# Performance work log

Measured on AMD Instinct MI355X. Metric: run time of the kernel, lower is better.

Reference implementation:

```python
import jax, jax.numpy as jnp
import numpy as np

B, L, D, N, NBLK = 16, 2048, 256, 64, 6  # 6 S4D layers: blocks 1,2,3,5 + 2 inner layers of FS4Ddeq


def setup_inputs() -> dict:
    key = jax.random.key(0)
    ks = jax.random.split(key, 12)
    x = jax.random.normal(ks[0], (B, L), dtype=jnp.float32)
    W_emb = jax.random.normal(ks[1], (1, D), dtype=jnp.float32) * 0.1
    b_emb = jnp.zeros((D,), jnp.float32)
    # S4D parameters, stacked over the 6 layers
    log_dt = jax.random.uniform(ks[2], (NBLK, D), minval=float(np.log(1e-3)), maxval=float(np.log(1e-1)), dtype=jnp.float32)
    logAre = jnp.full((NBLK, D, N), float(np.log(0.5)), jnp.float32)
    Aim = jnp.broadcast_to(jnp.pi * jnp.arange(N, dtype=jnp.float32), (NBLK, D, N)) * jnp.ones((NBLK, D, N), jnp.float32)
    Cre = jax.random.normal(ks[3], (NBLK, D, N), dtype=jnp.float32) * (0.5 ** 0.5)
    Cim = jax.random.normal(ks[4], (NBLK, D, N), dtype=jnp.float32) * (0.5 ** 0.5)
    Dskip = jax.random.normal(ks[5], (NBLK, D), dtype=jnp.float32)
    Wout = jax.random.normal(ks[6], (NBLK, D, D), dtype=jnp.float32) / np.sqrt(D)
    bout = jnp.zeros((NBLK, D), jnp.float32)
    gamma = jnp.ones((NBLK, D), jnp.float32)
    beta = jnp.zeros((NBLK, D), jnp.float32)
    # feedforward of the FS4Ddeq block (feed_size=[B,L,emb_dim], feed_act='relu')
    feed_W1 = jax.random.normal(ks[7], (D, D), dtype=jnp.float32) / np.sqrt(D)
    feed_b1 = jnp.zeros((D,), jnp.float32)
    feed_W2 = jax.random.normal(ks[8], (D, D), dtype=jnp.float32) / np.sqrt(D)
    feed_b2 = jnp.zeros((D,), jnp.float32)
    fc_W = jax.random.normal(ks[9], (D, 2), dtype=jnp.float32) / np.sqrt(D)
    fc_b = jnp.zeros((2,), jnp.float32)
    return dict(x=x, W_emb=W_emb, b_emb=b_emb, log_dt=log_dt, logAre=logAre, Aim=Aim,
                Cre=Cre, Cim=Cim, Dskip=Dskip, Wout=Wout, bout=bout, gamma=gamma, beta=beta,
                feed_W1=feed_W1, feed_b1=feed_b1, feed_W2=feed_W2, feed_b2=feed_b2,
                fc_W=fc_W, fc_b=fc_b)


def _s4d_block(h, log_dt, logAre, Aim, Cre, Cim, Dskip, Wout, bout, gamma, beta):
    """Pre-norm (BN eval-mode) -> diagonal SSM (ZOH, FFT conv) -> GELU -> Linear -> residual."""
    _, Lh, _ = h.shape
    z = gamma * h + beta  # BatchNorm in eval mode with identity running stats
    dt = jnp.exp(log_dt)[:, None]                      # [D,1]
    A = -jnp.exp(logAre) + 1j * Aim                    # [D,N] diagonal state matrix
    dtA = dt * A                                       # [D,N]
    C = (Cre + 1j * Cim) * (jnp.exp(dtA) - 1.0) / A    # ZOH-discretized C*B
    # Vandermonde kernel K[d,l] = 2*Re sum_n C[d,n] * exp(dtA[d,n])^l
    vand = jnp.exp(dtA[:, :, None] * jnp.arange(Lh, dtype=jnp.float32))  # [D,N,L]
    K = 2.0 * jnp.einsum('dn,dnl->dl', C, vand).real   # [D,L]
    u = jnp.transpose(z, (0, 2, 1))                    # [B,D,L]
    kf = jnp.fft.rfft(K, n=2 * Lh)
    uf = jnp.fft.rfft(u, n=2 * Lh)
    y = jnp.fft.irfft(uf * kf, n=2 * Lh)[..., :Lh]     # causal conv
    y = y + Dskip[:, None] * u                         # feedthrough D
    y = jax.nn.gelu(jnp.transpose(y, (0, 2, 1)))       # [B,L,D]
    y = jnp.einsum('bld,de->ble', y, Wout) + bout      # output projection
    return y + h                                       # skip connection


def reference(x, W_emb, b_emb, log_dt, logAre, Aim, Cre, Cim, Dskip, Wout, bout,
              gamma, beta, feed_W1, feed_b1, feed_W2, feed_b2, fc_W, fc_b):
    h = x[..., None] @ W_emb + b_emb  # nn.Linear(1, emb_dim): [B,L,D]
    # layers 1,2,3,5: S4D blocks (dropout is identity in eval mode)
    for i in range(4):
        h = _s4d_block(h, log_dt[i], logAre[i], Aim[i], Cre[i], Cim[i],
                       Dskip[i], Wout[i], bout[i], gamma[i], beta[i])
    # layer4: FS4Ddeq_model with layers=2 inner S4D blocks + relu feed net + final relu + skip
    r = h
    for i in (4, 5):
        h = _s4d_block(h, log_dt[i], logAre[i], Aim[i], Cre[i], Cim[i],
                       Dskip[i], Wout[i], bout[i], gamma[i], beta[i])
    h = jax.nn.relu(h @ feed_W1 + feed_b1) @ feed_W2 + feed_b2
    h = jax.nn.relu(h + r)
    mean_y = jnp.mean(h, axis=1)       # [B,D]
    logits = mean_y @ fc_W + fc_b      # [B,2]
    return logits
```

## Files before the change

kernel.cpp:

```cpp
#include <hip/hip_runtime.h>
#include <hip/hip_fp16.h>
#include <math.h>

#define B_ 16
#define L_ 2048
#define D_ 256
#define N_ 64
#define NBLK_ 6
#define LC_ 128
#define NC_ 16

typedef _Float16 half8 __attribute__((ext_vector_type(8)));
typedef float f32x4 __attribute__((ext_vector_type(4)));

__device__ __forceinline__ unsigned short f2h(float f) {
  _Float16 h = (_Float16)f;
  return *(unsigned short*)&h;
}
__device__ __forceinline__ float h2f(unsigned short u) {
  _Float16 h = *(_Float16*)&u;
  return (float)h;
}

__global__ __launch_bounds__(256) void prep_kernel(
    const float* __restrict__ x, const float* __restrict__ wemb,
    const float* __restrict__ bemb,
    const float* __restrict__ log_dt, const float* __restrict__ logAre,
    const float* __restrict__ Aim, const float* __restrict__ Cre,
    const float* __restrict__ Cim,
    const float* __restrict__ Wout, const float* __restrict__ fW1,
    const float* __restrict__ fW2,
    float* __restrict__ wbuf, float* __restrict__ c2buf,
    float* __restrict__ wlbuf, unsigned short* __restrict__ WT,
    unsigned short* __restrict__ H, unsigned short* __restrict__ UT,
    int* __restrict__ cnt) {
  __shared__ __align__(16) unsigned char ldsraw[17408];
  int bid = blockIdx.x;
  int tid = threadIdx.x;
  if (bid < 384) {
    if (bid == 0 && tid < 16) cnt[tid] = 0;
    int idx = bid * 256 + tid;
    if (idx < NBLK_ * D_ * N_) {
      int blk = idx >> 14;
      int rem = idx & 16383;
      int d = rem >> 6;
      int n = rem & 63;
      float dt   = expf(log_dt[blk * D_ + d]);
      float are  = -expf(logAre[idx]);
      float aim  = Aim[idx];
      float dtar = dt * are, dtai = dt * aim;
      float er = expf(dtar);
      float wr = er * cosf(dtai);
      float wi = er * sinf(dtai);
      float inv = 1.0f / (are * are + aim * aim);
      float wm1r = wr - 1.0f;
      float br = (wm1r * are + wi * aim) * inv;
      float bi2 = (wi * are - wm1r * aim) * inv;
      float crv = Cre[idx], civ = Cim[idx];
      float c2r = 2.0f * (crv * br - civ * bi2);
      float c2i = 2.0f * (crv * bi2 + civ * br);
      float eL = expf((float)LC_ * dtar);
      float angL = (float)LC_ * dtai;
      float* wb = wbuf + (size_t)((blk << 8) + d) * 128;
      wb[n] = wr; wb[64 + n] = wi;
      float* cb = c2buf + (size_t)((blk << 8) + d) * 128;
      cb[n] = c2r; cb[64 + n] = c2i;
      wlbuf[2 * idx] = eL * cosf(angL); wlbuf[2 * idx + 1] = eL * sinf(angL);
    }
  } else if (bid < 512) {
    float (*tile)[65] = (float (*)[65])ldsraw;
    int b2 = bid - 384;
    int wv = b2 >> 4;
    int tk = (b2 >> 2) & 3;
    int tn = b2 & 3;
    const float* src = (wv < 6) ? (Wout + (size_t)wv * 65536) : (wv == 6 ? fW1 : fW2);
    int r = tid >> 4;
    int c = (tid & 15) << 2;
    for (int rr = 0; rr < 64; rr += 16) {
      float4 v = *(const float4*)(src + (size_t)(tk * 64 + r + rr) * 256 + tn * 64 + c);
      tile[r + rr][c] = v.x; tile[r + rr][c + 1] = v.y;
      tile[r + rr][c + 2] = v.z; tile[r + rr][c + 3] = v.w;
    }
    __syncthreads();
    for (int rr = 0; rr < 64; rr += 16) {
      int n = r + rr;
      ushort4 o;
      o.x = f2h(tile[c + 0][n]); o.y = f2h(tile[c + 1][n]);
      o.z = f2h(tile[c + 2][n]); o.w = f2h(tile[c + 3][n]);
      *(ushort4*)(WT + (size_t)wv * 65536 + (size_t)(tn * 64 + n) * 256 + tk * 64 + c) = o;
    }
  } else {
    unsigned short (*lds)[136] = (unsigned short (*)[136])ldsraw;
    int bi = bid - 512;
    int bc = bi >> 2, dq = bi & 3;
    int b = bc >> 4, ch = bc & 15;
    int tau0 = tid >> 4;
    int dl = (tid & 15) << 2;
    float w4[4], b4[4];
#pragma unroll
    for (int i = 0; i < 4; ++i) {
      w4[i] = wemb[dq * 64 + dl + i];
      b4[i] = bemb[dq * 64 + dl + i];
    }
    for (int tt = 0; tt < 128; tt += 16) {
      int l = ch * 128 + tt + tau0;
      float xv = x[b * L_ + l];
      ushort4 hv;
      float v0 = fmaf(xv, w4[0], b4[0]);
      float v1 = fmaf(xv, w4[1], b4[1]);
      float v2 = fmaf(xv, w4[2], b4[2]);
      float v3 = fmaf(xv, w4[3], b4[3]);
      hv.x = f2h(v0); hv.y = f2h(v1); hv.z = f2h(v2); hv.w = f2h(v3);
      lds[dl + 0][tt + tau0] = hv.x;
      lds[dl + 1][tt + tau0] = hv.y;
      lds[dl + 2][tt + tau0] = hv.z;
      lds[dl + 3][tt + tau0] = hv.w;
      *(ushort4*)(H + ((size_t)(b * L_ + l)) * D_ + dq * 64 + dl) = hv;
    }
    __syncthreads();
    int r = tid >> 2, seg = (tid & 3) << 5;
    unsigned short* dst = UT + ((size_t)((dq * 64 + r) * 256 + bc)) * 128 + seg;
    const unsigned short* srow = &lds[r][seg];
    *(uint4*)(dst + 0)  = *(const uint4*)(srow + 0);
    *(uint4*)(dst + 8)  = *(const uint4*)(srow + 8);
    *(uint4*)(dst + 16) = *(const uint4*)(srow + 16);
    *(uint4*)(dst + 24) = *(const uint4*)(srow + 24);
  }
}

__global__ __launch_bounds__(512) void scan_fused(
    const unsigned short* __restrict__ UT,
    const float* __restrict__ WB, const float* __restrict__ C2B,
    const float* __restrict__ WLB,
    const float* __restrict__ gamma_, const float* __restrict__ beta_,
    const float* __restrict__ dskip,
    unsigned short* __restrict__ GT, int blk) {
  __shared__ __align__(16) unsigned short SLl[256 * 136];
  __shared__ __align__(16) unsigned short Bm1[128 * 136];
  __shared__ __align__(16) unsigned short Bm2[128 * 136];
  __shared__ float wc[256];
  __shared__ float Kt[128];
  __shared__ float Pb[128];
  __shared__ float Sb[128];
  int d = blockIdx.x;
  int tid = threadIdx.x, lane = tid & 63, w = tid >> 6;
  int wm = (w & 3) << 6;
  int wn = (w >> 2) << 6;
  int cn = lane & 15, rq = lane >> 4;
  int ko = rq << 3;
  const unsigned short* Au = UT + (size_t)d * 256 * 128;

  half8 afr[4][4];
#pragma unroll
  for (int kc2 = 0; kc2 < 4; ++kc2)
#pragma unroll
    for (int mf = 0; mf < 4; ++mf)
      afr[kc2][mf] = *(const half8*)(Au + (size_t)(wm + (mf << 4) + cn) * 128 + (kc2 << 5) + ko);

  if (tid < 128) wc[tid] = WB[(size_t)((blk << 8) + d) * 128 + tid];
  else if (tid < 256) wc[tid] = C2B[(size_t)((blk << 8) + d) * 128 + (tid - 128)];
  __syncthreads();
  int n = tid & 63;
  float gd = gamma_[blk * D_ + d], bd = beta_[blk * D_ + d], dsk = dskip[blk * D_ + d];
  {
    float wr = wc[n], wi = wc[64 + n];
    float c2r = wc[128 + n], c2i = wc[192 + n];
    int j0 = w << 4;
    float pr = 1.f, pi = 0.f, br = wr, bi = wi;
    int e = j0;
    while (e) {
      if (e & 1) { float tt = pr * br - pi * bi; pi = pr * bi + pi * br; pr = tt; }
      float t2 = br * br - bi * bi; bi = 2.f * br * bi; br = t2;
      e >>= 1;
    }
    for (int k2 = 0; k2 < 16; ++k2) {
      int j = j0 + k2;
      Bm1[n * 136 + (127 - j)]        = f2h(gd * pr);
      Bm1[(64 + n) * 136 + (127 - j)] = f2h(-gd * pi);
      float qr = pr * wr - pi * wi, qi = pr * wi + pi * wr;
      Bm2[j * 136 + n]      = f2h(c2r * qr - c2i * qi);
      Bm2[j * 136 + 64 + n] = f2h(c2r * qi + c2i * qr);
      float kc = c2r * pr - c2i * pi;
#pragma unroll
      for (int off = 1; off < 64; off <<= 1) kc += __shfl_xor(kc, off);
      if (n == 0) Kt[j] = kc + (j == 0 ? dsk : 0.f);
      pr = qr; pi = qi;
    }
  }
  if (tid < 64) {
    const float* wlp = WLB + (((size_t)((blk << 8) + d)) * 64 + tid) * 2;
    float wlr = wlp[0], wli = wlp[1];
    float nr = wlr - 1.f, ni = wli;
    float dr2 = wc[tid] - 1.f, di = wc[64 + tid];
    float iv = 1.f / (dr2 * dr2 + di * di);
    Sb[tid]      = bd * ((nr * dr2 + ni * di) * iv);
    Sb[64 + tid] = bd * (-((ni * dr2 - nr * di) * iv));
  }
  __syncthreads();

  {
    f32x4 acc[4][4];
#pragma unroll
    for (int a = 0; a < 4; ++a)
#pragma unroll
      for (int b2 = 0; b2 < 4; ++b2) acc[a][b2] = (f32x4){0.f, 0.f, 0.f, 0.f};
#pragma unroll
    for (int kc = 0; kc < 4; ++kc) {
      half8 bf4[4];
#pragma unroll
      for (int nf = 0; nf < 4; ++nf)
        bf4[nf] = *(const half8*)((const _Float16*)Bm1 + (wn + (nf << 4) + cn) * 136 + (kc << 5) + ko);
#pragma unroll
      for (int mf = 0; mf < 4; ++mf)
#pragma unroll
        for (int nf = 0; nf < 4; ++nf)
          acc[mf][nf] = __builtin_amdgcn_mfma_f32_16x16x32_f16(afr[kc][mf], bf4[nf], acc[mf][nf], 0, 0, 0);
    }
#pragma unroll
    for (int nf = 0; nf < 4; ++nf) {
      int nl = wn + (nf << 4) + cn;
      float sb = Sb[nl];
#pragma unroll
      for (int mf = 0; mf < 4; ++mf)
#pragma unroll
        for (int rr = 0; rr < 4; ++rr) {
          int row = wm + (mf << 4) + (rq << 2) + rr;
          SLl[row * 136 + nl] = f2h(acc[mf][nf][rr] + sb);
        }
    }
  }
  __syncthreads();

  if (tid < 128) {
    float ps = 0.f;
    for (int t2 = 0; t2 <= tid; ++t2) ps += Kt[t2];
    Pb[tid] = bd * ps;
  }
  for (int task = tid; task < 1024; task += 512) {
    int b = task >> 6, nn = task & 63;
    const float* wlp = WLB + (((size_t)((blk << 8) + d)) * 64 + nn) * 2;
    float wlr = wlp[0], wli = wlp[1];
    float Sr = 0.f, Sj = 0.f;
    int row0 = b << 4;
    float tr2 = h2f(SLl[row0 * 136 + nn]);
    float tj2 = h2f(SLl[row0 * 136 + 64 + nn]);
    for (int c = 0; c < NC_; ++c) {
      int row = row0 + c;
      float ntr = 0.f, ntj = 0.f;
      if (c < NC_ - 1) {
        ntr = h2f(SLl[(row + 1) * 136 + nn]);
        ntj = h2f(SLl[(row + 1) * 136 + 64 + nn]);
      }
      SLl[row * 136 + nn]      = f2h(Sr);
      SLl[row * 136 + 64 + nn] = f2h(Sj);
      float nSr = fmaf(wlr, Sr, fmaf(wli, Sj, tr2));
      Sj = fmaf(-wli, Sr, fmaf(wlr, Sj, tj2));
      Sr = nSr;
      tr2 = ntr; tj2 = ntj;
    }
  }
  __syncthreads();

  {
    int chunk = tid & 15, rg = tid >> 4;
#pragma unroll
    for (int it = 0; it < 4; ++it) {
      int trow = (it << 5) + rg;
      int tau0 = chunk << 3;
      unsigned short v[8];
#pragma unroll
      for (int i = 0; i < 8; ++i) {
        int tau = tau0 + i;
        v[i] = (tau <= trow) ? f2h(gd * Kt[trow - tau]) : (unsigned short)0;
      }
      *(uint4*)(Bm1 + (size_t)trow * 136 + tau0) = *(uint4*)v;
    }
  }
  __syncthreads();

  {
    f32x4 acc[4][4];
#pragma unroll
    for (int a = 0; a < 4; ++a)
#pragma unroll
      for (int b2 = 0; b2 < 4; ++b2) acc[a][b2] = (f32x4){0.f, 0.f, 0.f, 0.f};
#pragma unroll
    for (int kb = 0; kb < 8; ++kb) {
      int kc = (kb & 3) << 5;
      half8 af[4], bf4[4];
      if (kb < 4) {
#pragma unroll
        for (int mf = 0; mf < 4; ++mf) af[mf] = afr[kb][mf];
#pragma unroll
        for (int nf = 0; nf < 4; ++nf)
          bf4[nf] = *(const half8*)((const _Float16*)Bm1 + (wn + (nf << 4) + cn) * 136 + kc + ko);
      } else {
#pragma unroll
        for (int mf = 0; mf < 4; ++mf)
          af[mf] = *(const half8*)((const _Float16*)SLl + (wm + (mf << 4) + cn) * 136 + kc + ko);
#pragma unroll
        for (int nf = 0; nf < 4; ++nf)
          bf4[nf] = *(const half8*)((const _Float16*)Bm2 + (wn + (nf << 4) + cn) * 136 + kc + ko);
      }
#pragma unroll
      for (int mf = 0; mf < 4; ++mf)
#pragma unroll
        for (int nf = 0; nf < 4; ++nf)
          acc[mf][nf] = __builtin_amdgcn_mfma_f32_16x16x32_f16(af[mf], bf4[nf], acc[mf][nf], 0, 0, 0);
    }
    __syncthreads();
    unsigned short* epi = SLl;
#pragma unroll
    for (int nf = 0; nf < 4; ++nf) {
      int nl = wn + (nf << 4) + cn;
      float pb2 = Pb[nl];
#pragma unroll
      for (int mf = 0; mf < 4; ++mf)
#pragma unroll
        for (int rr = 0; rr < 4; ++rr) {
          int ml = wm + (mf << 4) + (rq << 2) + rr;
          float xx = acc[mf][nf][rr] + pb2;
          float x3 = xx * xx * xx;
          float inner = 0.7978845608028654f * fmaf(0.044715f, x3, xx);
          float e = __expf(-2.f * fabsf(inner));
          float th = (1.f - e) / (1.f + e);
          th = copysignf(th, inner);
          epi[ml * 136 + nl] = f2h(0.5f * xx * (1.f + th));
        }
    }
    __syncthreads();
    int mr = tid >> 1, hf = (tid & 1) << 6;
    size_t gb = ((size_t)d * 256 + mr) * 128 + hf;
#pragma unroll
    for (int k = 0; k < 8; ++k)
      *(uint4*)(GT + gb + k * 8) = *(const uint4*)&epi[mr * 136 + hf + k * 8];
  }
}

__global__ __launch_bounds__(256, 4) void gemm_gt(const unsigned short* __restrict__ GT,
    const unsigned short* __restrict__ Wt, const float* __restrict__ bias,
    const unsigned short* __restrict__ res, unsigned short* __restrict__ hout,
    unsigned short* __restrict__ ut_next) {
  __shared__ __align__(16) unsigned short smem[9216 + 4608];
  unsigned short* As = smem;
  unsigned short* Bs = smem + 9216;
  int tid = threadIdx.x;
  int bid = blockIdx.x;
  int bc = bid & 255;
  int m0 = bc << 7, n0 = (bid >> 8) << 6;
  int lane = tid & 63, w = tid >> 6;
  int wm = (w & 1) << 6, wn = (w >> 1) << 5;
  int rb = tid >> 3, cb = (tid & 7) << 3;
  int dr = tid >> 2, sg = (tid & 3) << 5;
  f32x4 acc[4][2];
#pragma unroll
  for (int mf = 0; mf < 4; ++mf)
#pragma unroll
    for (int nf = 0; nf < 2; ++nf) acc[mf][nf] = (f32x4){0.f, 0.f, 0.f, 0.f};

  uint4 gv[4], bv[2];
  {
    const uint4* grow = (const uint4*)(GT + ((size_t)(dr * 256 + bc)) * 128 + sg);
    gv[0] = grow[0]; gv[1] = grow[1]; gv[2] = grow[2]; gv[3] = grow[3];
#pragma unroll
    for (int rr = 0; rr < 2; ++rr)
      bv[rr] = *(const uint4*)(Wt + (size_t)(n0 + rb + rr * 32) * 256 + cb);
  }
  for (int kb = 0; kb < 4; ++kb) {
    __syncthreads();
    const unsigned short* pv = (const unsigned short*)gv;
#pragma unroll
    for (int i = 0; i < 32; ++i) As[(sg + i) * 72 + dr] = pv[i];
#pragma unroll
    for (int rr = 0; rr < 2; ++rr) *(uint4*)&Bs[(rb + rr * 32) * 72 + cb] = bv[rr];
    __syncthreads();
    if (kb < 3) {
      int k0 = (kb + 1) << 6;
      const uint4* grow = (const uint4*)(GT + ((size_t)((k0 + dr) * 256 + bc)) * 128 + sg);
      gv[0] = grow[0]; gv[1] = grow[1]; gv[2] = grow[2]; gv[3] = grow[3];
#pragma unroll
      for (int rr = 0; rr < 2; ++rr)
        bv[rr] = *(const uint4*)(Wt + (size_t)(n0 + rb + rr * 32) * 256 + k0 + cb);
    }
#pragma unroll
    for (int kw = 0; kw < 2; ++kw) {
      int ko = (kw << 5) + ((lane >> 4) << 3);
      half8 af[4], bfr[2];
#pragma unroll
      for (int mf = 0; mf < 4; ++mf)
        af[mf] = *(const half8*)&As[(wm + (mf << 4) + (lane & 15)) * 72 + ko];
#pragma unroll
      for (int nf = 0; nf < 2; ++nf)
        bfr[nf] = *(const half8*)&Bs[(wn + (nf << 4) + (lane & 15)) * 72 + ko];
#pragma unroll
      for (int mf = 0; mf < 4; ++mf)
#pragma unroll
        for (int nf = 0; nf < 2; ++nf)
          acc[mf][nf] = __builtin_amdgcn_mfma_f32_16x16x32_f16(af[mf], bfr[nf], acc[mf][nf], 0, 0, 0);
    }
  }
  int cn = lane & 15, rq = lane >> 4;
  __syncthreads();
  unsigned short* epi = smem;
#pragma unroll
  for (int nf = 0; nf < 2; ++nf) {
    int nl = wn + (nf << 4) + cn;
    float bv2 = bias[n0 + nl];
#pragma unroll
    for (int mf = 0; mf < 4; ++mf)
#pragma unroll
      for (int r = 0; r < 4; ++r) {
        int ml = wm + (mf << 4) + (rq << 2) + r;
        float v = acc[mf][nf][r] + bv2 + h2f(res[(size_t)(m0 + ml) * 256 + n0 + nl]);
        epi[ml * 72 + nl] = f2h(v);
      }
  }
  __syncthreads();
  {
    int mr = tid >> 1, hf = (tid & 1) << 5;
    unsigned short* dst = hout + (size_t)(m0 + mr) * 256 + n0 + hf;
    const unsigned short* srow = epi + mr * 72 + hf;
#pragma unroll
    for (int k = 0; k < 4; ++k) *(uint4*)(dst + k * 8) = *(const uint4*)(srow + k * 8);
  }
  if (ut_next) {
    int nl = tid >> 2, sg2 = (tid & 3) << 5;
    unsigned short* dst = ut_next + ((size_t)(n0 + nl) * 256 + bc) * 128 + sg2;
#pragma unroll
    for (int k = 0; k < 4; ++k) {
      unsigned short v8[8];
#pragma unroll
      for (int e = 0; e < 8; ++e) v8[e] = epi[(sg2 + k * 8 + e) * 72 + nl];
      *(uint4*)(dst + k * 8) = *(uint4*)v8;
    }
  }
}

__global__ __launch_bounds__(256, 4) void gemm_ffn(const unsigned short* __restrict__ A,
    const unsigned short* __restrict__ Wt, const float* __restrict__ bias,
    const unsigned short* __restrict__ res, unsigned short* __restrict__ outp) {
  __shared__ __align__(16) unsigned short smem[9216 + 4608];
  unsigned short* As = smem;
  unsigned short* Bs = smem + 9216;
  int tid = threadIdx.x;
  int bid = blockIdx.x;
  int m0 = (bid & 255) << 7, n0 = (bid >> 8) << 6;
  int lane = tid & 63, w = tid >> 6;
  int wm = (w & 1) << 6, wn = (w >> 1) << 5;
  int r0 = tid >> 3;
  int c0 = (tid & 7) << 3;
  f32x4 acc[4][2];
#pragma unroll
  for (int mf = 0; mf < 4; ++mf)
#pragma unroll
    for (int nf = 0; nf < 2; ++nf) acc[mf][nf] = (f32x4){0.f, 0.f, 0.f, 0.f};

  uint4 av[4], bv[2];
#pragma unroll
  for (int rr = 0; rr < 4; ++rr)
    av[rr] = *(const uint4*)(A + (size_t)(m0 + r0 + rr * 32) * 256 + c0);
#pragma unroll
  for (int rr = 0; rr < 2; ++rr)
    bv[rr] = *(const uint4*)(Wt + (size_t)(n0 + r0 + rr * 32) * 256 + c0);
  for (int kb = 0; kb < 4; ++kb) {
    __syncthreads();
#pragma unroll
    for (int rr = 0; rr < 4; ++rr) *(uint4*)&As[(r0 + rr * 32) * 72 + c0] = av[rr];
#pragma unroll
    for (int rr = 0; rr < 2; ++rr) *(uint4*)&Bs[(r0 + rr * 32) * 72 + c0] = bv[rr];
    __syncthreads();
    if (kb < 3) {
      int k0 = (kb + 1) << 6;
#pragma unroll
      for (int rr = 0; rr < 4; ++rr)
        av[rr] = *(const uint4*)(A + (size_t)(m0 + r0 + rr * 32) * 256 + k0 + c0);
#pragma unroll
      for (int rr = 0; rr < 2; ++rr)
        bv[rr] = *(const uint4*)(Wt + (size_t)(n0 + r0 + rr * 32) * 256 + k0 + c0);
    }
#pragma unroll
    for (int kw = 0; kw < 2; ++kw) {
      int ko = (kw << 5) + ((lane >> 4) << 3);
      half8 af[4], bfr[2];
#pragma unroll
      for (int mf = 0; mf < 4; ++mf)
        af[mf] = *(const half8*)&As[(wm + (mf << 4) + (lane & 15)) * 72 + ko];
#pragma unroll
      for (int nf = 0; nf < 2; ++nf)
        bfr[nf] = *(const half8*)&Bs[(wn + (nf << 4) + (lane & 15)) * 72 + ko];
#pragma unroll
      for (int mf = 0; mf < 4; ++mf)
#pragma unroll
        for (int nf = 0; nf < 2; ++nf)
          acc[mf][nf] = __builtin_amdgcn_mfma_f32_16x16x32_f16(af[mf], bfr[nf], acc[mf][nf], 0, 0, 0);
    }
  }
  int cn = lane & 15, rq = lane >> 4;
  __syncthreads();
  unsigned short* epi = smem;
#pragma unroll
  for (int nf = 0; nf < 2; ++nf) {
    int nl = wn + (nf << 4) + cn;
#pragma unroll
    for (int r = 0; r < 4; ++r) {
#pragma unroll
      for (int mf = 0; mf < 4; ++mf) {
        int ml = wm + (mf << 4) + (rq << 2) + r;
        epi[ml * 72 + nl] = f2h(acc[mf][nf][r]);
      }
    }
  }
  __syncthreads();
  int mr = tid >> 1, hf = (tid & 1) << 5;
  unsigned short* dst = outp + (size_t)(m0 + mr) * 256 + n0 + hf;
#pragma unroll
  for (int k = 0; k < 4; ++k) {
    uint4 c = *(const uint4*)&epi[mr * 72 + hf + k * 8];
    uint4 rv = (uint4){0, 0, 0, 0};
    if (res) rv = *(const uint4*)(res + (size_t)(m0 + mr) * 256 + n0 + hf + k * 8);
    const unsigned short* cp = (const unsigned short*)&c;
    const unsigned short* rp = (const unsigned short*)&rv;
    unsigned short o8[8];
#pragma unroll
    for (int e = 0; e < 8; ++e) {
      float v = h2f(cp[e]) + bias[n0 + hf + k * 8 + e];
      if (res) v += h2f(rp[e]);
      o8[e] = f2h(fmaxf(v, 0.f));
    }
    *(uint4*)(dst + k * 8) = *(uint4*)o8;
  }
}

__global__ __launch_bounds__(256) void head_kernel(const unsigned short* __restrict__ H,
    float* __restrict__ part, int* __restrict__ cnt,
    const float* __restrict__ fcW, const float* __restrict__ fcb,
    float* __restrict__ out) {
  __shared__ float meanv[D_];
  __shared__ int lastFlag;
  int b = blockIdx.x, ls = blockIdx.y, d = threadIdx.x;
  const unsigned short* p = H + ((size_t)(b * L_ + ls * 128)) * D_ + d;
  float sum = 0.f;
  for (int l = 0; l < 128; ++l) sum += h2f(p[(size_t)l * D_]);
  part[(b * 16 + ls) * D_ + d] = sum;
  __syncthreads();
  if (d == 0) {
    __threadfence();
    lastFlag = (atomicAdd(&cnt[b], 1) == 15) ? 1 : 0;
  }
  __syncthreads();
  if (lastFlag) {
    __threadfence();
    const volatile float* vp = part;
    float s = 0.f;
    for (int i = 0; i < 16; ++i) s += vp[(b * 16 + i) * D_ + d];
    meanv[d] = s * (1.0f / (float)L_);
    __syncthreads();
    if (d < 2) {
      float accv = fcb[d];
      for (int k = 0; k < D_; ++k) accv = fmaf(meanv[k], fcW[k * 2 + d], accv);
      out[b * 2 + d] = accv;
    }
  }
}

extern "C" void kernel_launch(void* const* d_in, const int* in_sizes, int n_in,
                              void* d_out, int out_size, void* d_ws, size_t ws_size,
                              hipStream_t stream) {
  const float* x      = (const float*)d_in[0];
  const float* W_emb  = (const float*)d_in[1];
  const float* b_emb  = (const float*)d_in[2];
  const float* log_dt = (const float*)d_in[3];
  const float* logAre = (const float*)d_in[4];
  const float* Aim    = (const float*)d_in[5];
  const float* Cre    = (const float*)d_in[6];
  const float* Cim    = (const float*)d_in[7];
  const float* Dskip  = (const float*)d_in[8];
  const float* Wout   = (const float*)d_in[9];
  const float* bout   = (const float*)d_in[10];
  const float* gamma_ = (const float*)d_in[11];
  const float* beta_  = (const float*)d_in[12];
  const float* fW1    = (const float*)d_in[13];
  const float* fb1    = (const float*)d_in[14];
  const float* fW2    = (const float*)d_in[15];
  const float* fb2    = (const float*)d_in[16];
  const float* fcW    = (const float*)d_in[17];
  const float* fcb    = (const float*)d_in[18];
  float* outp = (float*)d_out;

  const size_t HSZ = (size_t)B_ * L_ * D_;
  float* WB     = (float*)d_ws;
  float* C2B    = WB + (size_t)NBLK_ * D_ * 128;
  float* WLB    = C2B + (size_t)NBLK_ * D_ * 128;
  unsigned short* H   = (unsigned short*)(WLB + (size_t)NBLK_ * D_ * N_ * 2);
  unsigned short* R   = H + HSZ;
  unsigned short* UT  = R + HSZ;
  unsigned short* GT  = UT + HSZ;
  unsigned short* Gbf = GT;
  unsigned short* WT  = GT + HSZ;
  int* cnt = (int*)(WT + (size_t)8 * 65536);

  prep_kernel<<<1536, 256, 0, stream>>>(x, W_emb, b_emb, log_dt, logAre, Aim, Cre, Cim,
                                        Wout, fW1, fW2, WB, C2B, WLB, WT, H, UT, cnt);

  const unsigned short* hin_t[6]  = {H, H, H, H, R, H};
  unsigned short*       hout_t[6] = {H, H, H, R, H, H};
  for (int i = 0; i < 6; ++i) {
    scan_fused<<<256, 512, 0, stream>>>(UT, WB, C2B, WLB, gamma_, beta_, Dskip, GT, i);
    gemm_gt<<<1024, 256, 0, stream>>>(
        GT, WT + (size_t)i * 65536, bout + i * D_, hin_t[i], hout_t[i],
        (i < 5) ? UT : nullptr);
  }
  gemm_ffn<<<1024, 256, 0, stream>>>(H, WT + (size_t)6 * 65536, fb1, nullptr, Gbf);
  gemm_ffn<<<1024, 256, 0, stream>>>(Gbf, WT + (size_t)7 * 65536, fb2, R, H);
  head_kernel<<<dim3(16, 16), 256, 0, stream>>>(H, WB, cnt, fcW, fcb, outp);
}
```

Before: 538.6 us.

## Split scan_fused across two blocks per channel to halve LDS and double grid

Each channel's 256-row chunk matrix is now processed by two workgroups, each handling 128 rows (half the batch). Shared memory drops by merging Bm1/Bm2 into one reused buffer and halving SLl, and the output GEMMs are reordered so the state-contribution product is computed before the causal Toeplitz matrix overwrites the buffer. This lets more workgroups fit per CU and doubles the grid from 256 to 512 blocks to fill the GPU better. The cost is that per-channel setup (the power series, the kernel taps and their prefix sums) is recomputed in both blocks. It also adds s_setprio around the MFMA loops and a launch-bounds occupancy hint.

```diff
diff --git a/kernel.cpp b/kernel.cpp
--- a/kernel.cpp
+++ b/kernel.cpp
@@ -128,27 +128,28 @@
   }
 }
 
-__global__ __launch_bounds__(512) void scan_fused(
+__global__ __launch_bounds__(512, 4) void scan_fused(
     const unsigned short* __restrict__ UT,
     const float* __restrict__ WB, const float* __restrict__ C2B,
     const float* __restrict__ WLB,
     const float* __restrict__ gamma_, const float* __restrict__ beta_,
     const float* __restrict__ dskip,
     unsigned short* __restrict__ GT, int blk) {
-  __shared__ __align__(16) unsigned short SLl[256 * 136];
-  __shared__ __align__(16) unsigned short Bm1[128 * 136];
-  __shared__ __align__(16) unsigned short Bm2[128 * 136];
+  __shared__ __align__(16) unsigned short SLl[128 * 136];
+  __shared__ __align__(16) unsigned short Bm[128 * 136];
   __shared__ float wc[256];
   __shared__ float Kt[128];
   __shared__ float Pb[128];
   __shared__ float Sb[128];
-  int d = blockIdx.x;
+  int bid = blockIdx.x;
+  int d = bid >> 1;
+  int hm = (bid & 1) << 7;
   int tid = threadIdx.x, lane = tid & 63, w = tid >> 6;
-  int wm = (w & 3) << 6;
-  int wn = (w >> 2) << 6;
+  int wm = (w & 1) << 6;
+  int wn = (w >> 1) << 5;
   int cn = lane & 15, rq = lane >> 4;
   int ko = rq << 3;
-  const unsigned short* Au = UT + (size_t)d * 256 * 128;
+  const unsigned short* Au = UT + ((size_t)d * 256 + hm) * 128;
 
   half8 afr[4][4];
 #pragma unroll
@@ -162,10 +163,11 @@
   __syncthreads();
   int n = tid & 63;
   float gd = gamma_[blk * D_ + d], bd = beta_[blk * D_ + d], dsk = dskip[blk * D_ + d];
-  {
-    float wr = wc[n], wi = wc[64 + n];
-    float c2r = wc[128 + n], c2i = wc[192 + n];
-    int j0 = w << 4;
+  float wr = wc[n], wi = wc[64 + n];
+  float c2r = wc[128 + n], c2i = wc[192 + n];
+  float pr0, pi0;
+  int j0 = w << 4;
+  {
     float pr = 1.f, pi = 0.f, br = wr, bi = wi;
     int e = j0;
     while (e) {
@@ -173,13 +175,13 @@
       float t2 = br * br - bi * bi; bi = 2.f * br * bi; br = t2;
       e >>= 1;
     }
+    pr0 = pr; pi0 = pi;
+#pragma unroll 4
     for (int k2 = 0; k2 < 16; ++k2) {
       int j = j0 + k2;
-      Bm1[n * 136 + (127 - j)]        = f2h(gd * pr);
-      Bm1[(64 + n) * 136 + (127 - j)] = f2h(-gd * pi);
+      Bm[n * 136 + (127 - j)]        = f2h(gd * pr);
+      Bm[(64 + n) * 136 + (127 - j)] = f2h(-gd * pi);
       float qr = pr * wr - pi * wi, qi = pr * wi + pi * wr;
-      Bm2[j * 136 + n]      = f2h(c2r * qr - c2i * qi);
-      Bm2[j * 136 + 64 + n] = f2h(c2r * qi + c2i * qr);
       float kc = c2r * pr - c2i * pi;
 #pragma unroll
       for (int off = 1; off < 64; off <<= 1) kc += __shfl_xor(kc, off);
@@ -199,25 +201,27 @@
   __syncthreads();
 
   {
-    f32x4 acc[4][4];
+    f32x4 acc[4][2];
 #pragma unroll
     for (int a = 0; a < 4; ++a)
 #pragma unroll
-      for (int b2 = 0; b2 < 4; ++b2) acc[a][b2] = (f32x4){0.f, 0.f, 0.f, 0.f};
+      for (int b2 = 0; b2 < 2; ++b2) acc[a][b2] = (f32x4){0.f, 0.f, 0.f, 0.f};
+    __builtin_amdgcn_s_setprio(1);
 #pragma unroll
     for (int kc = 0; kc < 4; ++kc) {
-      half8 bf4[4];
-#pragma unroll
-      for (int nf = 0; nf < 4; ++nf)
-        bf4[nf] = *(const half8*)((const _Float16*)Bm1 + (wn + (nf << 4) + cn) * 136 + (kc << 5) + ko);
-#pragma unroll
-      for (int mf = 0; mf < 4; ++mf)
-#pragma unroll
-        for (int nf = 0; nf < 4; ++nf)
+      half8 bf4[2];
+#pragma unroll
+      for (int nf = 0; nf < 2; ++nf)
+        bf4[nf] = *(const half8*)((const _Float16*)Bm + (wn + (nf << 4) + cn) * 136 + (kc << 5) + ko);
+#pragma unroll
+      for (int mf = 0; mf < 4; ++mf)
+#pragma unroll
+        for (int nf = 0; nf < 2; ++nf)
           acc[mf][nf] = __builtin_amdgcn_mfma_f32_16x16x32_f16(afr[kc][mf], bf4[nf], acc[mf][nf], 0, 0, 0);
     }
-#pragma unroll
-    for (int nf = 0; nf < 4; ++nf) {
+    __builtin_amdgcn_s_setprio(0);
+#pragma unroll
+    for (int nf = 0; nf < 2; ++nf) {
       int nl = wn + (nf << 4) + cn;
       float sb = Sb[nl];
 #pragma unroll
@@ -231,13 +235,24 @@
   }
   __syncthreads();
 
+  {
+    float pr = pr0, pi = pi0;
+#pragma unroll 4
+    for (int k2 = 0; k2 < 16; ++k2) {
+      int j = j0 + k2;
+      float qr = pr * wr - pi * wi, qi = pr * wi + pi * wr;
+      Bm[j * 136 + n]      = f2h(c2r * qr - c2i * qi);
+      Bm[j * 136 + 64 + n] = f2h(c2r * qi + c2i * qr);
+      pr = qr; pi = qi;
+    }
+  }
   if (tid < 128) {
     float ps = 0.f;
     for (int t2 = 0; t2 <= tid; ++t2) ps += Kt[t2];
     Pb[tid] = bd * ps;
   }
-  for (int task = tid; task < 1024; task += 512) {
-    int b = task >> 6, nn = task & 63;
+  {
+    int b = tid >> 6, nn = tid & 63;
     const float* wlp = WLB + (((size_t)((blk << 8) + d)) * 64 + nn) * 2;
     float wlr = wlp[0], wli = wlp[1];
     float Sr = 0.f, Sj = 0.f;
@@ -261,6 +276,31 @@
   }
   __syncthreads();
 
+  f32x4 acc3[4][2];
+#pragma unroll
+  for (int a = 0; a < 4; ++a)
+#pragma unroll
+    for (int b2 = 0; b2 < 2; ++b2) acc3[a][b2] = (f32x4){0.f, 0.f, 0.f, 0.f};
+  __builtin_amdgcn_s_setprio(1);
+#pragma unroll
+  for (int kc2 = 0; kc2 < 4; ++kc2) {
+    int kc = kc2 << 5;
+    half8 af[4], bf4[2];
+#pragma unroll
+    for (int mf = 0; mf < 4; ++mf)
+      af[mf] = *(const half8*)((const _Float16*)SLl + (wm + (mf << 4) + cn) * 136 + kc + ko);
+#pragma unroll
+    for (int nf = 0; nf < 2; ++nf)
+      bf4[nf] = *(const half8*)((const _Float16*)Bm + (wn + (nf << 4) + cn) * 136 + kc + ko);
+#pragma unroll
+    for (int mf = 0; mf < 4; ++mf)
+#pragma unroll
+      for (int nf = 0; nf < 2; ++nf)
+        acc3[mf][nf] = __builtin_amdgcn_mfma_f32_16x16x32_f16(af[mf], bf4[nf], acc3[mf][nf], 0, 0, 0);
+  }
+  __builtin_amdgcn_s_setprio(0);
+  __syncthreads();
+
   {
     int chunk = tid & 15, rg = tid >> 4;
 #pragma unroll
@@ -273,45 +313,28 @@
         int tau = tau0 + i;
         v[i] = (tau <= trow) ? f2h(gd * Kt[trow - tau]) : (unsigned short)0;
       }
-      *(uint4*)(Bm1 + (size_t)trow * 136 + tau0) = *(uint4*)v;
-    }
-  }
-  __syncthreads();
-
-  {
-    f32x4 acc[4][4];
-#pragma unroll
-    for (int a = 0; a < 4; ++a)
-#pragma unroll
-      for (int b2 = 0; b2 < 4; ++b2) acc[a][b2] = (f32x4){0.f, 0.f, 0.f, 0.f};
-#pragma unroll
-    for (int kb = 0; kb < 8; ++kb) {
-      int kc = (kb & 3) << 5;
-      half8 af[4], bf4[4];
-      if (kb < 4) {
-#pragma unroll
-        for (int mf = 0; mf < 4; ++mf) af[mf] = afr[kb][mf];
-#pragma unroll
-        for (int nf = 0; nf < 4; ++nf)
-          bf4[nf] = *(const half8*)((const _Float16*)Bm1 + (wn + (nf << 4) + cn) * 136 + kc + ko);
-      } else {
-#pragma unroll
-        for (int mf = 0; mf < 4; ++mf)
-          af[mf] = *(const half8*)((const _Float16*)SLl + (wm + (mf << 4) + cn) * 136 + kc + ko);
-#pragma unroll
-        for (int nf = 0; nf < 4; ++nf)
-          bf4[nf] = *(const half8*)((const _Float16*)Bm2 + (wn + (nf << 4) + cn) * 136 + kc + ko);
-      }
-#pragma unroll
-      for (int mf = 0; mf < 4; ++mf)
-#pragma unroll
-        for (int nf = 0; nf < 4; ++nf)
-          acc[mf][nf] = __builtin_amdgcn_mfma_f32_16x16x32_f16(af[mf], bf4[nf], acc[mf][nf], 0, 0, 0);
-    }
-    __syncthreads();
-    unsigned short* epi = SLl;
-#pragma unroll
-    for (int nf = 0; nf < 4; ++nf) {
+      *(uint4*)(Bm + (size_t)trow * 136 + tau0) = *(uint4*)v;
+    }
+  }
+  __syncthreads();
+
+  {
+    __builtin_amdgcn_s_setprio(1);
+#pragma unroll
+    for (int kc2 = 0; kc2 < 4; ++kc2) {
+      half8 bf4[2];
+#pragma unroll
+      for (int nf = 0; nf < 2; ++nf)
+        bf4[nf] = *(const half8*)((const _Float16*)Bm + (wn + (nf << 4) + cn) * 136 + (kc2 << 5) + ko);
+#pragma unroll
+      for (int mf = 0; mf < 4; ++mf)
+#pragma unroll
+        for (int nf = 0; nf < 2; ++nf)
+          acc3[mf][nf] = __builtin_amdgcn_mfma_f32_16x16x32_f16(afr[kc2][mf], bf4[nf], acc3[mf][nf], 0, 0, 0);
+    }
+    __builtin_amdgcn_s_setprio(0);
+#pragma unroll
+    for (int nf = 0; nf < 2; ++nf) {
       int nl = wn + (nf << 4) + cn;
       float pb2 = Pb[nl];
 #pragma unroll
@@ -319,21 +342,21 @@
 #pragma unroll
         for (int rr = 0; rr < 4; ++rr) {
           int ml = wm + (mf << 4) + (rq << 2) + rr;
-          float xx = acc[mf][nf][rr] + pb2;
+          float xx = acc3[mf][nf][rr] + pb2;
           float x3 = xx * xx * xx;
           float inner = 0.7978845608028654f * fmaf(0.044715f, x3, xx);
           float e = __expf(-2.f * fabsf(inner));
           float th = (1.f - e) / (1.f + e);
           th = copysignf(th, inner);
-          epi[ml * 136 + nl] = f2h(0.5f * xx * (1.f + th));
+          SLl[ml * 136 + nl] = f2h(0.5f * xx * (1.f + th));
         }
     }
     __syncthreads();
-    int mr = tid >> 1, hf = (tid & 1) << 6;
-    size_t gb = ((size_t)d * 256 + mr) * 128 + hf;
-#pragma unroll
-    for (int k = 0; k < 8; ++k)
-      *(uint4*)(GT + gb + k * 8) = *(const uint4*)&epi[mr * 136 + hf + k * 8];
+    int mr = tid >> 2, hf = (tid & 3) << 5;
+    size_t gb = ((size_t)d * 256 + hm + mr) * 128 + hf;
+#pragma unroll
+    for (int k = 0; k < 4; ++k)
+      *(uint4*)(GT + gb + k * 8) = *(const uint4*)&SLl[mr * 136 + hf + k * 8];
   }
 }
 
@@ -605,7 +628,7 @@
   const unsigned short* hin_t[6]  = {H, H, H, H, R, H};
   unsigned short*       hout_t[6] = {H, H, H, R, H, H};
   for (int i = 0; i < 6; ++i) {
-    scan_fused<<<256, 512, 0, stream>>>(UT, WB, C2B, WLB, gamma_, beta_, Dskip, GT, i);
+    scan_fused<<<512, 512, 0, stream>>>(UT, WB, C2B, WLB, gamma_, beta_, Dskip, GT, i);
     gemm_gt<<<1024, 256, 0, stream>>>(
         GT, WT + (size_t)i * 65536, bout + i * D_, hin_t[i], hout_t[i],
         (i < 5) ? UT : nullptr);
```

Result: slower. 551.1 us (+2.3%).
